# Kernel optimization log

Hardware: AMD Instinct MI355X
Metric: run time of the kernel (lower is better)

## Reference

```python
import jax, jax.numpy as jnp
import numpy as np

jax.config.update("jax_enable_x64", True)

EPS = 1e-3
MAX_EIG = 1000.0


def setup_inputs() -> dict:
    key = jax.random.key(0)
    a = jax.random.normal(key, (4096, 64, 64), dtype=jnp.float32)
    # symmetrize so input is a valid symmetric matrix (eigvals then clamped to SPD)
    x = 0.5 * (a + jnp.swapaxes(a, -1, -2))
    return {"x": x}


def _clamp_recon(x64, transform):
    # eigh in fp64, clamp eigvals, apply transform, reconstruct V diag(f(w)) V^T
    w, v = jnp.linalg.eigh(x64)
    w = transform(jnp.clip(w, EPS, MAX_EIG))
    return (v * w[..., None, :]) @ jnp.swapaxes(v, -1, -2)


def reference(x) -> jnp.ndarray:
    # safe_eigh: fp64 eigh, clamp eigvals to [eps, max_eig], reconstruct, cast fp32
    x_spd = _clamp_recon(x.astype(jnp.float64), lambda w: w).astype(jnp.float32)
    # matrix log: fp64 eigh again, clamp, log eigvals, reconstruct, cast fp32
    x_log = _clamp_recon(x_spd.astype(jnp.float64), jnp.log).astype(jnp.float32)
    return x_log
```

## Files before the change

### kernel.cpp

```cpp
#include <hip/hip_runtime.h>
#include <math.h>

#define MIN_SWEEPS 6
#define MAX_SWEEPS 9
#define EPSV 1e-3
#define MAXEIG 1000.0


#define REP64(X) \
  X(0) X(1) X(2) X(3) X(4) X(5) X(6) X(7) \
  X(8) X(9) X(10) X(11) X(12) X(13) X(14) X(15) \
  X(16) X(17) X(18) X(19) X(20) X(21) X(22) X(23) \
  X(24) X(25) X(26) X(27) X(28) X(29) X(30) X(31) \
  X(32) X(33) X(34) X(35) X(36) X(37) X(38) X(39) \
  X(40) X(41) X(42) X(43) X(44) X(45) X(46) X(47) \
  X(48) X(49) X(50) X(51) X(52) X(53) X(54) X(55) \
  X(56) X(57) X(58) X(59) X(60) X(61) X(62) X(63)

__global__ __launch_bounds__(64, 2)
void spd_log_kernel(const float* __restrict__ x, float* __restrict__ out) {
    __shared__ float vlds[64 * 65];

    const int lane = (int)threadIdx.x;
    const size_t mat = blockIdx.x;
    const float* __restrict__ xm = x + mat * (size_t)4096;
    float* __restrict__ om = out + mat * (size_t)4096;

#define DECLW(i) float w##i;
    REP64(DECLW)
#define DECLQ(i) float q##i;
    REP64(DECLQ)

#define LOADW(i) w##i = xm[(i) * 64 + lane];
    REP64(LOADW)

    float ff = 0.0f;
#define ACCF(i) ff = fmaf(w##i, w##i, ff);
    REP64(ACCF)
#pragma unroll
    for (int o = 32; o > 0; o >>= 1) ff += __shfl_xor(ff, o);
    const float gamma = 0.5f * sqrtf(ff);

#define SHIFTW(i) w##i += ((i) == lane) ? gamma : 0.0f;
    REP64(SHIFTW)

    float n = 0.0f;
#define ACCN(i) n = fmaf(w##i, w##i, n);
    REP64(ACCN)

    for (int sweep = 0; sweep < MAX_SWEEPS; ++sweep) {
        n = 0.0f;
        REP64(ACCN)
        float S = n;
#pragma unroll
        for (int o = 32; o > 0; o >>= 1) S += __shfl_xor(S, o);
        float off2 = 0.0f;

        for (int m = 1; m < 64; ++m) {
            const int pidx = ((lane ^ m) << 2);
#define FETCH(i) q##i = __int_as_float(__builtin_amdgcn_ds_bpermute(pidx, __float_as_int(w##i)));
            REP64(FETCH)
            float g = 0.0f;
#define ACCG(i) g = fmaf(w##i, q##i, g);
            REP64(ACCG)
            off2 = fmaf(g, g, off2);
            const float nq = __int_as_float(__builtin_amdgcn_ds_bpermute(pidx, __float_as_int(n)));
            const bool isp = lane < (lane ^ m);
            const float na = isp ? n : nq;
            const float nb = isp ? nq : n;
            const float tau = (nb - na) * (0.5f * __builtin_amdgcn_rcpf(g));
            const float at  = fabsf(tau);
            float t = __builtin_amdgcn_rcpf(at + __builtin_amdgcn_sqrtf(fmaf(at, at, 1.0f)));
            t = copysignf(t, tau);
            float c = __builtin_amdgcn_rsqf(fmaf(t, t, 1.0f));
            float s = t * c;
            const bool tiny = !(fabsf(g) > 1e-28f);
            c = tiny ? 1.0f : c;
            s = tiny ? 0.0f : s;
            const float tg = tiny ? 0.0f : t * g;
            const float se = isp ? -s : s;
#define ROT(i) w##i = fmaf(se, q##i, c * w##i);
            REP64(ROT)
            n += isp ? -tg : tg;
        }
#pragma unroll
        for (int o = 32; o > 0; o >>= 1) off2 += __shfl_xor(off2, o);
        if (sweep >= MIN_SWEEPS - 1 && off2 < 1e-13f * S * S) break;
    }

    n = 0.0f;
    REP64(ACCN)
    const float rn = __builtin_amdgcn_rsqf(n);
#define NRM(i) w##i *= rn;
    REP64(NRM)

#define DUMP(i) vlds[lane * 65 + (i)] = w##i;
    REP64(DUMP)
    __syncthreads();

    double acc = 0.0;
    for (int r = 0; r < 64; ++r) {
        double inner = 0.0;
#define RAY(i) inner = fma((double)xm[r * 64 + (i)], (double)w##i, inner);
        REP64(RAY)
        const float vr = vlds[lane * 65 + r];
        acc = fma((double)vr, inner, acc);
    }
    double lam = fmin(fmax(acc, (double)EPSV), (double)MAXEIG);
    const float f = (float)log(lam);

#define G2(i) q##i = __uint_as_float(__builtin_amdgcn_readlane(__float_as_uint(f), (i))) * vlds[(i) * 65 + lane];
    REP64(G2)

    for (int r = 0; r < 64; ++r) {
        float a = 0.0f;
#define REC(i) a = fmaf(vlds[(i) * 65 + r], q##i, a);
        REP64(REC)
        om[r * 64 + lane] = a;
    }
}

extern "C" void kernel_launch(void* const* d_in, const int* in_sizes, int n_in,
                              void* d_out, int out_size, void* d_ws, size_t ws_size,
                              hipStream_t stream) {
    const float* x = (const float*)d_in[0];
    float* out = (float*)d_out;
    const int nmat = in_sizes[0] / 4096;
    spd_log_kernel<<<dim3(nmat), dim3(64), 0, stream>>>(x, out);
}
```

Before: 1.702 ms.

## Relax launch bounds, halve LDS epilogue buffer, split Jacobi dot-product accumulators

```diff
diff --git a/kernel.cpp b/kernel.cpp
--- a/kernel.cpp
+++ b/kernel.cpp
@@ -17,11 +17,19 @@
   X(48) X(49) X(50) X(51) X(52) X(53) X(54) X(55) \
   X(56) X(57) X(58) X(59) X(60) X(61) X(62) X(63)
 
-__global__ __launch_bounds__(64, 2)
+#define REP32(X) \
+  X(0) X(1) X(2) X(3) X(4) X(5) X(6) X(7) \
+  X(8) X(9) X(10) X(11) X(12) X(13) X(14) X(15) \
+  X(16) X(17) X(18) X(19) X(20) X(21) X(22) X(23) \
+  X(24) X(25) X(26) X(27) X(28) X(29) X(30) X(31)
+
+__global__ __launch_bounds__(64)
 void spd_log_kernel(const float* __restrict__ x, float* __restrict__ out) {
-    __shared__ float vlds[64 * 65];
+    __shared__ float vlds[32 * 65];
 
     const int lane = (int)threadIdx.x;
+    const int hb   = lane >> 5;
+    const int rl   = lane & 31;
     const size_t mat = blockIdx.x;
     const float* __restrict__ xm = x + mat * (size_t)4096;
     float* __restrict__ om = out + mat * (size_t)4096;
@@ -60,9 +68,11 @@
             const int pidx = ((lane ^ m) << 2);
 #define FETCH(i) q##i = __int_as_float(__builtin_amdgcn_ds_bpermute(pidx, __float_as_int(w##i)));
             REP64(FETCH)
-            float g = 0.0f;
-#define ACCG(i) g = fmaf(w##i, q##i, g);
+            float gp[8] = {0.f, 0.f, 0.f, 0.f, 0.f, 0.f, 0.f, 0.f};
+#define ACCG(i) gp[(i) & 7] = fmaf(w##i, q##i, gp[(i) & 7]);
             REP64(ACCG)
+            const float g = ((gp[0] + gp[1]) + (gp[2] + gp[3])) +
+                            ((gp[4] + gp[5]) + (gp[6] + gp[7]));
             off2 = fmaf(g, g, off2);
             const float nq = __int_as_float(__builtin_amdgcn_ds_bpermute(pidx, __float_as_int(n)));
             const bool isp = lane < (lane ^ m);
@@ -94,29 +104,40 @@
 #define NRM(i) w##i *= rn;
     REP64(NRM)
 
-#define DUMP(i) vlds[lane * 65 + (i)] = w##i;
-    REP64(DUMP)
-    __syncthreads();
+    float f = 0.0f;
 
-    double acc = 0.0;
-    for (int r = 0; r < 64; ++r) {
-        double inner = 0.0;
-#define RAY(i) inner = fma((double)xm[r * 64 + (i)], (double)w##i, inner);
-        REP64(RAY)
-        const float vr = vlds[lane * 65 + r];
-        acc = fma((double)vr, inner, acc);
-    }
-    double lam = fmin(fmax(acc, (double)EPSV), (double)MAXEIG);
-    const float f = (float)log(lam);
+#pragma unroll
+    for (int P = 0; P < 2; ++P) {
+        __syncthreads();
+        if (hb == P) {
+#define DUMP(i) vlds[rl * 65 + (i)] = w##i;
+            REP64(DUMP)
+        }
+        __syncthreads();
 
-#define G2(i) q##i = __uint_as_float(__builtin_amdgcn_readlane(__float_as_uint(f), (i))) * vlds[(i) * 65 + lane];
-    REP64(G2)
+        if (hb == P) {
+            double acc = 0.0;
+            for (int r = 0; r < 64; ++r) {
+                double ip[4] = {0.0, 0.0, 0.0, 0.0};
+#define RAYI(i) ip[(i) >> 4] = fma((double)xm[r * 64 + (i)], (double)w##i, ip[(i) >> 4]);
+                REP64(RAYI)
+                const double inner = (ip[0] + ip[1]) + (ip[2] + ip[3]);
+                acc = fma((double)vlds[rl * 65 + r], inner, acc);
+            }
+            double lam = fmin(fmax(acc, (double)EPSV), (double)MAXEIG);
+            f = (float)log(lam);
+        }
 
-    for (int r = 0; r < 64; ++r) {
-        float a = 0.0f;
-#define REC(i) a = fmaf(vlds[(i) * 65 + r], q##i, a);
-        REP64(REC)
-        om[r * 64 + lane] = a;
+#define G2(i) q##i = __uint_as_float(__builtin_amdgcn_readlane(__float_as_uint(f), 32 * P + (i))) * vlds[(i) * 65 + lane];
+        REP32(G2)
+
+        for (int r = 0; r < 64; ++r) {
+            float a = 0.0f;
+#define RECI(i) a = fmaf(vlds[(i) * 65 + r], q##i, a);
+            REP32(RECI)
+            if (P == 0) om[r * 64 + lane] = a;
+            else        om[r * 64 + lane] += a;
+        }
     }
 }
 
```

Measured after the change: 2.382 ms. 1.4x slower.
